# Performance work log

Measured on AMD Instinct MI355X. Metric: run time of the kernel, lower is better.

The kernel has to match this reference:

```python
import jax, jax.numpy as jnp
import numpy as np
import math

B, S, H = 2, 2048, 1024
NH = 16
HD = H // NH  # 64


def setup_inputs() -> dict:
    key = jax.random.key(0)
    ks = jax.random.split(key, 8)
    scale = 1.0 / math.sqrt(H)
    inp = {
        "hidden_states": jax.random.normal(ks[0], (B, S, H), dtype=jnp.float32),
        "attention_mask": jnp.zeros((B, 1, 1, S), dtype=jnp.float32),
        "Wq": jax.random.normal(ks[1], (H, H), dtype=jnp.float32) * scale,
        "bq": jnp.zeros((H,), dtype=jnp.float32),
        "Wk": jax.random.normal(ks[2], (H, H), dtype=jnp.float32) * scale,
        "bk": jnp.zeros((H,), dtype=jnp.float32),
        "Wv": jax.random.normal(ks[3], (H, H), dtype=jnp.float32) * scale,
        "bv": jnp.zeros((H,), dtype=jnp.float32),
    }
    return inp


def reference(hidden_states, attention_mask, Wq, bq, Wk, bk, Wv, bv):
    # torch Linear: y = x @ W.T + b; W is (out, in)
    def split_heads(x):  # [B,S,H] -> [B,NH,S,HD]
        return x.reshape(B, S, NH, HD).transpose(0, 2, 1, 3)

    q = split_heads(hidden_states @ Wq.T + bq)
    k = split_heads(hidden_states @ Wk.T + bk)
    v = split_heads(hidden_states @ Wv.T + bv)

    scores = jnp.einsum('bhqd,bhkd->bhqk', q, k) / jnp.sqrt(jnp.float32(HD))
    scores = scores + attention_mask  # additive mask, broadcast [B,1,1,S]
    probs = jax.nn.softmax(scores, axis=-1)
    # dropout prob = 0.0 -> identity
    ctx = jnp.einsum('bhqk,bhkd->bhqd', probs, v)
    ctx = ctx.transpose(0, 2, 1, 3).reshape(B, S, H)
    return ctx
```

## Files before the change

kernel.cpp:

```cpp
#include <hip/hip_runtime.h>
#include <hip/hip_bf16.h>
#include <stdint.h>

constexpr int cB = 2;
constexpr int cS = 2048;
constexpr int cH = 1024;
constexpr int cNH = 16;
constexpr int cHD = 64;
constexpr int cBS = cB * cS;

typedef short short8 __attribute__((ext_vector_type(8)));
typedef short short4v __attribute__((ext_vector_type(4)));
typedef float f32x4 __attribute__((ext_vector_type(4)));

__device__ inline unsigned short f2bf(float f) {
  __hip_bfloat16 h = __float2bfloat16(f);
  return __builtin_bit_cast(unsigned short, h);
}

__device__ inline void gload_lds16(const void* g, void* l) {
  __builtin_amdgcn_global_load_lds(
      (const __attribute__((address_space(1))) void*)g,
      (__attribute__((address_space(3))) void*)l,
      16, 0, 0);
}

__device__ inline short4v tr16(const unsigned short* p) {
  short4v d;
  auto p3 = (const __attribute__((address_space(3))) unsigned short*)p;
  asm volatile("ds_read_b64_tr_b16 %0, %1" : "=v"(d) : "v"(p3) : "memory");
  return d;
}

template <int CTRL>
__device__ inline float dppmax(float x) {
  int v = __builtin_bit_cast(int, x);
  int y = __builtin_amdgcn_update_dpp(0, v, CTRL, 0xf, 0xf, true);
  return fmaxf(x, __builtin_bit_cast(float, y));
}

__device__ inline float rowmax16(float x) {
  x = dppmax<0x121>(x);
  x = dppmax<0x122>(x);
  x = dppmax<0x124>(x);
  x = dppmax<0x128>(x);
  return x;
}

constexpr int BM = 128, BN = 128, BK = 32;

__global__ __launch_bounds__(256) void qkv_gemm(
    const float* __restrict__ X,
    const float* __restrict__ Wq,
    const float* __restrict__ Wk,
    const float* __restrict__ Wv,
    const float* __restrict__ bq, const float* __restrict__ bk,
    const float* __restrict__ bv,
    unsigned short* __restrict__ Qb, unsigned short* __restrict__ Kb,
    unsigned short* __restrict__ Vb) {
  __shared__ alignas(16) unsigned short As[BM * BK];
  __shared__ alignas(16) unsigned short Bs[BN * BK];

  const int nb = blockIdx.x;
  const int mb = blockIdx.y;
  const int m0 = mb * BM;
  const int wsel = nb >> 3;
  const int n0 = (nb & 7) * BN;
  const float* W = (wsel == 0) ? Wq : (wsel == 1 ? Wk : Wv);
  const float* bias = (wsel == 0) ? bq : (wsel == 1 ? bk : bv);
  unsigned short* Out = (wsel == 0) ? Qb : (wsel == 1 ? Kb : Vb);
  const float oscale = (wsel == 0) ? 0.125f : 1.0f;

  const int t = threadIdx.x;
  const int w = t >> 6, l = t & 63, lr = l & 15, lg = l >> 4;
  const int wm = w >> 1, wn = w & 1;
  const int srow = t >> 1;
  const int scol = (t & 1) * 16;

  f32x4 acc[4][4];
#pragma unroll
  for (int mi = 0; mi < 4; ++mi)
#pragma unroll
    for (int ni = 0; ni < 4; ++ni) acc[mi][ni] = {0.f, 0.f, 0.f, 0.f};

  for (int kt = 0; kt < cH / BK; ++kt) {
    const int k0 = kt * BK;
    __syncthreads();
    {
      const float* s = X + (size_t)(m0 + srow) * cH + k0 + scol;
      f32x4 v0 = *reinterpret_cast<const f32x4*>(s);
      f32x4 v1 = *reinterpret_cast<const f32x4*>(s + 4);
      f32x4 v2 = *reinterpret_cast<const f32x4*>(s + 8);
      f32x4 v3 = *reinterpret_cast<const f32x4*>(s + 12);
      short8 o0, o1;
#pragma unroll
      for (int j = 0; j < 4; ++j) {
        o0[j] = (short)f2bf(v0[j]);
        o0[4 + j] = (short)f2bf(v1[j]);
        o1[j] = (short)f2bf(v2[j]);
        o1[4 + j] = (short)f2bf(v3[j]);
      }
      *reinterpret_cast<short8*>(&As[srow * BK + scol]) = o0;
      *reinterpret_cast<short8*>(&As[srow * BK + scol + 8]) = o1;
    }
    {
      const float* s = W + (size_t)(n0 + srow) * cH + k0 + scol;
      f32x4 v0 = *reinterpret_cast<const f32x4*>(s);
      f32x4 v1 = *reinterpret_cast<const f32x4*>(s + 4);
      f32x4 v2 = *reinterpret_cast<const f32x4*>(s + 8);
      f32x4 v3 = *reinterpret_cast<const f32x4*>(s + 12);
      short8 o0, o1;
#pragma unroll
      for (int j = 0; j < 4; ++j) {
        o0[j] = (short)f2bf(v0[j]);
        o0[4 + j] = (short)f2bf(v1[j]);
        o1[j] = (short)f2bf(v2[j]);
        o1[4 + j] = (short)f2bf(v3[j]);
      }
      *reinterpret_cast<short8*>(&Bs[srow * BK + scol]) = o0;
      *reinterpret_cast<short8*>(&Bs[srow * BK + scol + 8]) = o1;
    }
    __syncthreads();

    short8 af[4], bfr[4];
#pragma unroll
    for (int mi = 0; mi < 4; ++mi)
      af[mi] = *reinterpret_cast<const short8*>(
          &As[(wm * 64 + mi * 16 + lr) * BK + lg * 8]);
#pragma unroll
    for (int ni = 0; ni < 4; ++ni)
      bfr[ni] = *reinterpret_cast<const short8*>(
          &Bs[(wn * 64 + ni * 16 + lr) * BK + lg * 8]);
#pragma unroll
    for (int mi = 0; mi < 4; ++mi)
#pragma unroll
      for (int ni = 0; ni < 4; ++ni)
        acc[mi][ni] = __builtin_amdgcn_mfma_f32_16x16x32_bf16(
            af[mi], bfr[ni], acc[mi][ni], 0, 0, 0);
  }

#pragma unroll
  for (int ni = 0; ni < 4; ++ni) {
    const int col = n0 + wn * 64 + ni * 16 + lr;
    const float bvv = bias[col];
#pragma unroll
    for (int mi = 0; mi < 4; ++mi) {
      const int row = m0 + wm * 64 + mi * 16 + lg * 4;
#pragma unroll
      for (int r = 0; r < 4; ++r)
        Out[(size_t)(row + r) * cH + col] =
            f2bf((acc[mi][ni][r] + bvv) * oscale);
    }
  }
}

__global__ __launch_bounds__(256) void attn_kernel(
    const unsigned short* __restrict__ Qb,
    const unsigned short* __restrict__ Kb,
    const unsigned short* __restrict__ Vb,
    const float* __restrict__ mask,
    float* __restrict__ out) {
  __shared__ alignas(16) unsigned short Ks[2][64 * 64];
  __shared__ alignas(16) unsigned short Vs[2][64 * 64];
  __shared__ alignas(16) unsigned short plds[4][2][64 * 16];

  const int qb = blockIdx.x;
  const int bh = blockIdx.y;
  const int b = bh >> 4, h = bh & 15;
  const int t = threadIdx.x;
  const int w = t >> 6, l = t & 63, lr = l & 15, lg = l >> 4;
  const int q0 = qb * 128 + w * 32;

  const unsigned short* Kbase = Kb + (size_t)b * cS * cH + h * cHD;
  const unsigned short* Vbase = Vb + (size_t)b * cS * cH + h * cHD;
  const float* mbase = mask + b * cS;

  int rK[2], cK[2], rV[2], cV[2];
#pragma unroll
  for (int s2 = 0; s2 < 2; ++s2) {
    const int g = (w * 2 + s2) * 64 + l;
    const int gr = g >> 3, gc = g & 7;
    rK[s2] = gr;
    cK[s2] = (gc ^ (gr & 7)) * 8;
    rV[s2] = (gr >> 2) * 4 + (gc >> 1);
    cV[s2] = (gr & 3) * 16 + (gc & 1) * 8;
  }

  short8 qf[2][2];
#pragma unroll
  for (int qi = 0; qi < 2; ++qi) {
    const unsigned short* Qrow =
        Qb + (size_t)(b * cS + q0 + qi * 16 + lr) * cH + h * cHD;
    qf[qi][0] = *reinterpret_cast<const short8*>(Qrow + lg * 8);
    qf[qi][1] = *reinterpret_cast<const short8*>(Qrow + 32 + lg * 8);
  }

  short8 ones;
#pragma unroll
  for (int j = 0; j < 8; ++j) ones[j] = (short)0x3F80;

  f32x4 oacc[2][4];
  f32x4 osum[2];
  float mrow[2][4];
#pragma unroll
  for (int qi = 0; qi < 2; ++qi) {
    osum[qi] = {0.f, 0.f, 0.f, 0.f};
#pragma unroll
    for (int d16 = 0; d16 < 4; ++d16) oacc[qi][d16] = {0.f, 0.f, 0.f, 0.f};
#pragma unroll
    for (int r = 0; r < 4; ++r) mrow[qi][r] = -1e30f;
  }

  auto stage = [&](int bufi, int kv0) {
#pragma unroll
    for (int s2 = 0; s2 < 2; ++s2) {
      gload_lds16(Kbase + (size_t)(kv0 + rK[s2]) * cH + cK[s2],
                  (char*)&Ks[bufi][0] + (w * 2 + s2) * 1024);
      gload_lds16(Vbase + (size_t)(kv0 + rV[s2]) * cH + cV[s2],
                  (char*)&Vs[bufi][0] + (w * 2 + s2) * 1024);
    }
  };

  stage(0, 0);
  asm volatile("s_waitcnt vmcnt(0)" ::: "memory");
  __syncthreads();

  unsigned short* pw0 = &plds[w][0][0];
  unsigned short* pw1 = &plds[w][1][0];

  constexpr int NT = cS / 64;
  for (int kt = 0; kt < NT; ++kt) {
    const int bufi = kt & 1;
    if (kt + 1 < NT) stage(bufi ^ 1, (kt + 1) * 64);

    const unsigned short* Kt = &Ks[bufi][0];
    const unsigned short* Vt = &Vs[bufi][0];
    const int kv0 = kt * 64;

    float mv[4];
#pragma unroll
    for (int n = 0; n < 4; ++n) mv[n] = mbase[kv0 + n * 16 + lr];

    f32x4 sc[2][4];
#pragma unroll
    for (int n = 0; n < 4; ++n) {
      const int kr = n * 16 + lr;
      const unsigned sw = (unsigned)((kr & 7) << 4);
      const unsigned b0 = ((unsigned)(kr * 128 + lg * 16)) ^ sw;
      const unsigned b1 = ((unsigned)(kr * 128 + 64 + lg * 16)) ^ sw;
      short8 kf0 = *reinterpret_cast<const short8*>((const char*)Kt + b0);
      short8 kf1 = *reinterpret_cast<const short8*>((const char*)Kt + b1);
#pragma unroll
      for (int qi = 0; qi < 2; ++qi) {
        f32x4 z = {0.f, 0.f, 0.f, 0.f};
        z = __builtin_amdgcn_mfma_f32_16x16x32_bf16(qf[qi][0], kf0, z, 0, 0, 0);
        z = __builtin_amdgcn_mfma_f32_16x16x32_bf16(qf[qi][1], kf1, z, 0, 0, 0);
        sc[qi][n] = z + mv[n];
      }
    }

    float mnew[2][4];
    int ok = 1;
#pragma unroll
    for (int qi = 0; qi < 2; ++qi)
#pragma unroll
      for (int r = 0; r < 4; ++r) {
        float mx = fmaxf(fmaxf(sc[qi][0][r], sc[qi][1][r]),
                         fmaxf(sc[qi][2][r], sc[qi][3][r]));
        mx = rowmax16(mx);
        mnew[qi][r] = fmaxf(mrow[qi][r], mx);
        ok &= (mx - mrow[qi][r] <= 8.0f) ? 1 : 0;
      }
    if (!__all(ok)) {
#pragma unroll
      for (int qi = 0; qi < 2; ++qi) {
#pragma unroll
        for (int r = 0; r < 4; ++r) {
          const float scalef = __expf(mrow[qi][r] - mnew[qi][r]);
          mrow[qi][r] = mnew[qi][r];
          osum[qi][r] *= scalef;
#pragma unroll
          for (int d16 = 0; d16 < 4; ++d16) oacc[qi][d16][r] *= scalef;
        }
      }
    }

#pragma unroll
    for (int qi = 0; qi < 2; ++qi) {
      unsigned short* pw = qi ? pw1 : pw0;
      const int pcb = (lg ^ (lr >> 2)) * 4;
#pragma unroll
      for (int n = 0; n < 4; ++n) {
        short4v v4;
#pragma unroll
        for (int r = 0; r < 4; ++r)
          v4[r] = (short)f2bf(__expf(sc[qi][n][r] - mrow[qi][r]));
        *reinterpret_cast<short4v*>(&pw[(n * 16 + lr) * 16 + pcb]) = v4;
      }
    }
    asm volatile("s_waitcnt lgkmcnt(0)" ::: "memory");
    __builtin_amdgcn_sched_barrier(0);

    short4v pt[2][4];
    short4v tv[2][8];
#pragma unroll
    for (int ks2 = 0; ks2 < 2; ++ks2) {
      const int k0 = ks2 * 32 + lg * 8;
      const int key = (lg & 1) * 2;
      pt[ks2][0] = tr16(&pw0[(k0 + (lr >> 2)) * 16 + (((lr & 3) ^ key) * 4)]);
      pt[ks2][1] =
          tr16(&pw0[(k0 + 4 + (lr >> 2)) * 16 + (((lr & 3) ^ key ^ 1) * 4)]);
      pt[ks2][2] = tr16(&pw1[(k0 + (lr >> 2)) * 16 + (((lr & 3) ^ key) * 4)]);
      pt[ks2][3] =
          tr16(&pw1[(k0 + 4 + (lr >> 2)) * 16 + (((lr & 3) ^ key ^ 1) * 4)]);
#pragma unroll
      for (int d16 = 0; d16 < 4; ++d16) {
        const unsigned short* a0 =
            Vt + (ks2 * 8 + lg * 2) * 256 + d16 * 64 + lr * 4;
        tv[ks2][2 * d16] = tr16(a0);
        tv[ks2][2 * d16 + 1] = tr16(a0 + 256);
      }
    }
    asm volatile("s_waitcnt lgkmcnt(0)" ::: "memory");
    __builtin_amdgcn_sched_barrier(0);
#pragma unroll
    for (int ks2 = 0; ks2 < 2; ++ks2) {
      short8 paA, paB;
#pragma unroll
      for (int j = 0; j < 4; ++j) {
        paA[j] = pt[ks2][0][j];
        paA[4 + j] = pt[ks2][1][j];
        paB[j] = pt[ks2][2][j];
        paB[4 + j] = pt[ks2][3][j];
      }
      osum[0] =
          __builtin_amdgcn_mfma_f32_16x16x32_bf16(paA, ones, osum[0], 0, 0, 0);
      osum[1] =
          __builtin_amdgcn_mfma_f32_16x16x32_bf16(paB, ones, osum[1], 0, 0, 0);
#pragma unroll
      for (int d16 = 0; d16 < 4; ++d16) {
        short8 vf;
#pragma unroll
        for (int j = 0; j < 4; ++j) {
          vf[j] = tv[ks2][2 * d16][j];
          vf[4 + j] = tv[ks2][2 * d16 + 1][j];
        }
        oacc[0][d16] = __builtin_amdgcn_mfma_f32_16x16x32_bf16(
            paA, vf, oacc[0][d16], 0, 0, 0);
        oacc[1][d16] = __builtin_amdgcn_mfma_f32_16x16x32_bf16(
            paB, vf, oacc[1][d16], 0, 0, 0);
      }
    }

    asm volatile("s_waitcnt vmcnt(0)" ::: "memory");
    __syncthreads();
  }

#pragma unroll
  for (int qi = 0; qi < 2; ++qi) {
    float* obase =
        out + (size_t)(b * cS + q0 + qi * 16 + lg * 4) * cH + h * cHD;
#pragma unroll
    for (int r = 0; r < 4; ++r) {
      const float inv = 1.0f / osum[qi][r];
#pragma unroll
      for (int d16 = 0; d16 < 4; ++d16)
        obase[(size_t)r * cH + d16 * 16 + lr] = oacc[qi][d16][r] * inv;
    }
  }
}

extern "C" void kernel_launch(void* const* d_in, const int* in_sizes, int n_in,
                              void* d_out, int out_size, void* d_ws,
                              size_t ws_size, hipStream_t stream) {
  const float* X = (const float*)d_in[0];
  const float* mask = (const float*)d_in[1];
  const float* Wq = (const float*)d_in[2];
  const float* bq = (const float*)d_in[3];
  const float* Wk = (const float*)d_in[4];
  const float* bk = (const float*)d_in[5];
  const float* Wv = (const float*)d_in[6];
  const float* bv = (const float*)d_in[7];
  float* outp = (float*)d_out;

  char* ws = (char*)d_ws;
  const size_t MB = 1 << 20;
  unsigned short* Qb = (unsigned short*)(ws + 0 * MB);
  unsigned short* Kb = (unsigned short*)(ws + 8 * MB);
  unsigned short* Vb = (unsigned short*)(ws + 16 * MB);

  qkv_gemm<<<dim3(24, 32), 256, 0, stream>>>(X, Wq, Wk, Wv, bq, bk, bv, Qb, Kb,
                                             Vb);
  attn_kernel<<<dim3(16, 32), 256, 0, stream>>>(Qb, Kb, Vb, mask, outp);
}
```

Before: 145.7 us.

## Pre-convert inputs to bf16, use direct-to-LDS loads in GEMM, switch softmax to exp2

Adds separate kernels that convert X and the three weight matrices to bf16 in workspace. The QKV GEMM then stages tiles with global_load_lds straight into shared memory, with no per-iteration conversion. The attention softmax moves to base-2 by folding log2(e) into the Q scale and the mask, seeds the MFMA accumulator with the mask, and raises the lazy-rescale threshold to match. The cost is four extra kernel launches and an extra round trip through global memory for the bf16 copies.

Measured after the change: 150.9 us. 1.04x slower.

```diff
diff --git a/kernel.cpp b/kernel.cpp
--- a/kernel.cpp
+++ b/kernel.cpp
@@ -12,11 +12,16 @@
 typedef short short8 __attribute__((ext_vector_type(8)));
 typedef short short4v __attribute__((ext_vector_type(4)));
 typedef float f32x4 __attribute__((ext_vector_type(4)));
+typedef unsigned short us4 __attribute__((ext_vector_type(4)));
+
+constexpr float LOG2E = 1.4426950408889634f;
 
 __device__ inline unsigned short f2bf(float f) {
   __hip_bfloat16 h = __float2bfloat16(f);
   return __builtin_bit_cast(unsigned short, h);
 }
+
+__device__ inline float fexp2(float x) { return exp2f(x); }
 
 __device__ inline void gload_lds16(const void* g, void* l) {
   __builtin_amdgcn_global_load_lds(
@@ -47,13 +52,22 @@
   return x;
 }
 
+__global__ void cvt_f32_bf16(const float* __restrict__ src,
+                             unsigned short* __restrict__ dst, int n) {
+  int i = (blockIdx.x * blockDim.x + threadIdx.x) * 4;
+  if (i >= n) return;
+  f32x4 v = *reinterpret_cast<const f32x4*>(src + i);
+  us4 o = {f2bf(v[0]), f2bf(v[1]), f2bf(v[2]), f2bf(v[3])};
+  *reinterpret_cast<us4*>(dst + i) = o;
+}
+
 constexpr int BM = 128, BN = 128, BK = 32;
 
 __global__ __launch_bounds__(256) void qkv_gemm(
-    const float* __restrict__ X,
-    const float* __restrict__ Wq,
-    const float* __restrict__ Wk,
-    const float* __restrict__ Wv,
+    const unsigned short* __restrict__ Xb,
+    const unsigned short* __restrict__ Wqb,
+    const unsigned short* __restrict__ Wkb,
+    const unsigned short* __restrict__ Wvb,
     const float* __restrict__ bq, const float* __restrict__ bk,
     const float* __restrict__ bv,
     unsigned short* __restrict__ Qb, unsigned short* __restrict__ Kb,
@@ -66,60 +80,37 @@
   const int m0 = mb * BM;
   const int wsel = nb >> 3;
   const int n0 = (nb & 7) * BN;
-  const float* W = (wsel == 0) ? Wq : (wsel == 1 ? Wk : Wv);
+  const unsigned short* W = (wsel == 0) ? Wqb : (wsel == 1 ? Wkb : Wvb);
   const float* bias = (wsel == 0) ? bq : (wsel == 1 ? bk : bv);
   unsigned short* Out = (wsel == 0) ? Qb : (wsel == 1 ? Kb : Vb);
-  const float oscale = (wsel == 0) ? 0.125f : 1.0f;
+  const float oscale = (wsel == 0) ? 0.125f * LOG2E : 1.0f;
 
   const int t = threadIdx.x;
   const int w = t >> 6, l = t & 63, lr = l & 15, lg = l >> 4;
   const int wm = w >> 1, wn = w & 1;
-  const int srow = t >> 1;
-  const int scol = (t & 1) * 16;
 
   f32x4 acc[4][4];
 #pragma unroll
   for (int mi = 0; mi < 4; ++mi)
 #pragma unroll
     for (int ni = 0; ni < 4; ++ni) acc[mi][ni] = {0.f, 0.f, 0.f, 0.f};
+
+  const int tb = t * 16;
 
   for (int kt = 0; kt < cH / BK; ++kt) {
     const int k0 = kt * BK;
     __syncthreads();
-    {
-      const float* s = X + (size_t)(m0 + srow) * cH + k0 + scol;
-      f32x4 v0 = *reinterpret_cast<const f32x4*>(s);
-      f32x4 v1 = *reinterpret_cast<const f32x4*>(s + 4);
-      f32x4 v2 = *reinterpret_cast<const f32x4*>(s + 8);
-      f32x4 v3 = *reinterpret_cast<const f32x4*>(s + 12);
-      short8 o0, o1;
-#pragma unroll
-      for (int j = 0; j < 4; ++j) {
-        o0[j] = (short)f2bf(v0[j]);
-        o0[4 + j] = (short)f2bf(v1[j]);
-        o1[j] = (short)f2bf(v2[j]);
-        o1[4 + j] = (short)f2bf(v3[j]);
-      }
-      *reinterpret_cast<short8*>(&As[srow * BK + scol]) = o0;
-      *reinterpret_cast<short8*>(&As[srow * BK + scol + 8]) = o1;
-    }
-    {
-      const float* s = W + (size_t)(n0 + srow) * cH + k0 + scol;
-      f32x4 v0 = *reinterpret_cast<const f32x4*>(s);
-      f32x4 v1 = *reinterpret_cast<const f32x4*>(s + 4);
-      f32x4 v2 = *reinterpret_cast<const f32x4*>(s + 8);
-      f32x4 v3 = *reinterpret_cast<const f32x4*>(s + 12);
-      short8 o0, o1;
-#pragma unroll
-      for (int j = 0; j < 4; ++j) {
-        o0[j] = (short)f2bf(v0[j]);
-        o0[4 + j] = (short)f2bf(v1[j]);
-        o1[j] = (short)f2bf(v2[j]);
-        o1[4 + j] = (short)f2bf(v3[j]);
-      }
-      *reinterpret_cast<short8*>(&Bs[srow * BK + scol]) = o0;
-      *reinterpret_cast<short8*>(&Bs[srow * BK + scol + 8]) = o1;
-    }
+#pragma unroll
+    for (int s = 0; s < 2; ++s) {
+      const int ib = s * 4096 + tb;
+      const int row = ib >> 6;
+      const int cole = (ib & 63) >> 1;
+      gload_lds16(Xb + (size_t)(m0 + row) * cH + k0 + cole,
+                  ((char*)As) + s * 4096 + w * 1024);
+      gload_lds16(W + (size_t)(n0 + row) * cH + k0 + cole,
+                  ((char*)Bs) + s * 4096 + w * 1024);
+    }
+    asm volatile("s_waitcnt vmcnt(0)" ::: "memory");
     __syncthreads();
 
     short8 af[4], bfr[4];
@@ -239,7 +230,7 @@
 
     float mv[4];
 #pragma unroll
-    for (int n = 0; n < 4; ++n) mv[n] = mbase[kv0 + n * 16 + lr];
+    for (int n = 0; n < 4; ++n) mv[n] = mbase[kv0 + n * 16 + lr] * LOG2E;
 
     f32x4 sc[2][4];
 #pragma unroll
@@ -252,10 +243,10 @@
       short8 kf1 = *reinterpret_cast<const short8*>((const char*)Kt + b1);
 #pragma unroll
       for (int qi = 0; qi < 2; ++qi) {
-        f32x4 z = {0.f, 0.f, 0.f, 0.f};
+        f32x4 z = {mv[n], mv[n], mv[n], mv[n]};
         z = __builtin_amdgcn_mfma_f32_16x16x32_bf16(qf[qi][0], kf0, z, 0, 0, 0);
         z = __builtin_amdgcn_mfma_f32_16x16x32_bf16(qf[qi][1], kf1, z, 0, 0, 0);
-        sc[qi][n] = z + mv[n];
+        sc[qi][n] = z;
       }
     }
 
@@ -269,14 +260,14 @@
                          fmaxf(sc[qi][2][r], sc[qi][3][r]));
         mx = rowmax16(mx);
         mnew[qi][r] = fmaxf(mrow[qi][r], mx);
-        ok &= (mx - mrow[qi][r] <= 8.0f) ? 1 : 0;
+        ok &= (mx - mrow[qi][r] <= 11.5416f) ? 1 : 0;
       }
     if (!__all(ok)) {
 #pragma unroll
       for (int qi = 0; qi < 2; ++qi) {
 #pragma unroll
         for (int r = 0; r < 4; ++r) {
-          const float scalef = __expf(mrow[qi][r] - mnew[qi][r]);
+          const float scalef = fexp2(mrow[qi][r] - mnew[qi][r]);
           mrow[qi][r] = mnew[qi][r];
           osum[qi][r] *= scalef;
 #pragma unroll
@@ -294,7 +285,7 @@
         short4v v4;
 #pragma unroll
         for (int r = 0; r < 4; ++r)
-          v4[r] = (short)f2bf(__expf(sc[qi][n][r] - mrow[qi][r]));
+          v4[r] = (short)f2bf(fexp2(sc[qi][n][r] - mrow[qi][r]));
         *reinterpret_cast<short4v*>(&pw[(n * 16 + lr) * 16 + pcb]) = v4;
       }
     }
@@ -385,11 +376,20 @@
 
   char* ws = (char*)d_ws;
   const size_t MB = 1 << 20;
-  unsigned short* Qb = (unsigned short*)(ws + 0 * MB);
-  unsigned short* Kb = (unsigned short*)(ws + 8 * MB);
-  unsigned short* Vb = (unsigned short*)(ws + 16 * MB);
-
-  qkv_gemm<<<dim3(24, 32), 256, 0, stream>>>(X, Wq, Wk, Wv, bq, bk, bv, Qb, Kb,
-                                             Vb);
+  unsigned short* Xb  = (unsigned short*)(ws + 0 * MB);
+  unsigned short* Wqb = (unsigned short*)(ws + 8 * MB);
+  unsigned short* Wkb = (unsigned short*)(ws + 10 * MB);
+  unsigned short* Wvb = (unsigned short*)(ws + 12 * MB);
+  unsigned short* Qb  = (unsigned short*)(ws + 14 * MB);
+  unsigned short* Kb  = (unsigned short*)(ws + 22 * MB);
+  unsigned short* Vb  = (unsigned short*)(ws + 30 * MB);
+
+  cvt_f32_bf16<<<cBS * cH / 1024, 256, 0, stream>>>(X, Xb, cBS * cH);
+  cvt_f32_bf16<<<cH * cH / 1024, 256, 0, stream>>>(Wq, Wqb, cH * cH);
+  cvt_f32_bf16<<<cH * cH / 1024, 256, 0, stream>>>(Wk, Wkb, cH * cH);
+  cvt_f32_bf16<<<cH * cH / 1024, 256, 0, stream>>>(Wv, Wvb, cH * cH);
+
+  qkv_gemm<<<dim3(24, 32), 256, 0, stream>>>(Xb, Wqb, Wkb, Wvb, bq, bk, bv,
+                                             Qb, Kb, Vb);
   attn_kernel<<<dim3(16, 32), 256, 0, stream>>>(Qb, Kb, Vb, mask, outp);
 }
```
